# Kernel optimization log

Measured on AMD Instinct MI355X. Metric: run time of the kernel, lower is better.

The kernel has to match this reference:

```python
import math
import jax, jax.numpy as jnp
import numpy as np

B, S, D, H = 4, 2048, 768, 8


def setup_inputs() -> dict:
    key = jax.random.key(0)
    ks = jax.random.split(key, 8)
    x = jax.random.normal(ks[0], (B, S, D), dtype=jnp.float32)
    # padding mask: True = masked position, shape [B, S, 1] as consumed by forward
    attention_mask = jax.random.randint(ks[1], (B, S, 1), 0, 2) == 1
    W_q = jax.random.normal(ks[2], (D, D), dtype=jnp.float32) * 0.02
    b_q = jax.random.normal(ks[3], (D,), dtype=jnp.float32) * 0.02
    W_v = jax.random.normal(ks[4], (D, D), dtype=jnp.float32) * 0.02
    b_v = jax.random.normal(ks[5], (D,), dtype=jnp.float32) * 0.02
    gamma = jnp.ones((D,), dtype=jnp.float32)
    beta = jnp.zeros((D,), dtype=jnp.float32)
    return {"x": x, "attention_mask": attention_mask, "W_q": W_q, "b_q": b_q,
            "W_v": W_v, "b_v": b_v, "gamma": gamma, "beta": beta}


def reference(x, attention_mask, W_q, b_q, W_v, b_v, gamma, beta):
    b, s, d = x.shape
    dk = d // H
    scale = math.sqrt(dk)
    q = (x @ W_q.T + b_q).reshape(b, s, H, dk).transpose(0, 2, 1, 3)  # [B,H,S,dk]
    # faithful to source: k and v BOTH use the V projection (original bug)
    kv = (x @ W_v.T + b_v).reshape(b, s, H, dk).transpose(0, 2, 1, 3)
    k = kv
    v = kv
    weight = jnp.einsum('bhid,bhjd->bhij', q, k) / scale  # [B,H,S,S]
    pad = attention_mask[:, None, :, :]                   # [B,1,S,1] -> broadcast over heads, j
    causal = jnp.triu(jnp.ones((s, s), dtype=bool), 1)    # [S,S]
    mask = pad | causal
    weight = jnp.where(mask, jnp.float32(-1e9), weight)
    # faithful: softmax over dim=2 (the query axis), as in the source
    score = jax.nn.softmax(weight, axis=2)
    out = jnp.einsum('bhij,bhjd->bhid', score, v)         # [B,H,S,dk]
    out = out.transpose(0, 2, 1, 3).reshape(b, s, d)
    out = out + x                                          # residual
    mu = jnp.mean(out, axis=-1, keepdims=True)
    var = jnp.mean((out - mu) ** 2, axis=-1, keepdims=True)
    return (out - mu) / jnp.sqrt(var + 1e-5) * gamma + beta
```

## Files before the change

### kernel.cpp

```cpp
#include <hip/hip_runtime.h>

#define B 4
#define S 2048
#define D 768
#define H 8
#define DK 96
#define NBH (B*H)
#define SD (B*S*D)

typedef __bf16 bf16x8 __attribute__((ext_vector_type(8)));
typedef float f32x4 __attribute__((ext_vector_type(4)));
typedef unsigned short ushort_t;
typedef __attribute__((ext_vector_type(8))) unsigned short ushort8;
typedef __attribute__((ext_vector_type(4))) unsigned short us4;

static constexpr float NEG = -1.0e9f;
static constexpr float SCALE_L2E = 0.14724515567714155f;

__device__ __forceinline__ float exp2v(float x) { return __builtin_amdgcn_exp2f(x); }

__device__ __forceinline__ ushort_t f2bf(float f) {
    union { float f; unsigned u; } v; v.f = f;
    unsigned r = v.u + 0x7fffu + ((v.u >> 16) & 1u);
    return (ushort_t)(r >> 16);
}

__device__ __forceinline__ unsigned cvt_pk(float a, float b) {
    unsigned d;
    asm("v_cvt_pk_bf16_f32 %0, %1, %2" : "=v"(d) : "v"(a), "v"(b));
    return d;
}
__device__ __forceinline__ ushort8 pack8(const float4& a, const float4& b) {
    union { unsigned u[4]; ushort8 s; } r;
    r.u[0] = cvt_pk(a.x, a.y); r.u[1] = cvt_pk(a.z, a.w);
    r.u[2] = cvt_pk(b.x, b.y); r.u[3] = cvt_pk(b.z, b.w);
    return r.s;
}
__device__ __forceinline__ us4 pack4(const float4& a) {
    union { unsigned u[2]; us4 s; } r;
    r.u[0] = cvt_pk(a.x, a.y); r.u[1] = cvt_pk(a.z, a.w);
    return r.s;
}

#define MFMA16(a, b, c) __builtin_amdgcn_mfma_f32_16x16x32_bf16((a), (b), (c), 0, 0, 0)

__global__ __launch_bounds__(256) void convert_bf16(
    const float* __restrict__ wq, const float* __restrict__ wv,
    ushort_t* __restrict__ wqb, ushort_t* __restrict__ wvb)
{
    const int stride = gridDim.x * 256;
    const int idx = blockIdx.x * 256 + threadIdx.x;
    for (int i = idx; i < (D * D) / 4; i += stride) {
        ((us4*)wqb)[i] = pack4(((const float4*)wq)[i]);
        ((us4*)wvb)[i] = pack4(((const float4*)wv)[i]);
    }
}

__global__ __launch_bounds__(256) void in_proj_gemm(
    const float* __restrict__ x,
    const ushort_t* __restrict__ wqb, const float* __restrict__ bq,
    const ushort_t* __restrict__ wvb, const float* __restrict__ bv,
    ushort_t* __restrict__ Qb, ushort_t* __restrict__ KVb,
    ushort_t* __restrict__ KVt)
{
    const ushort_t* __restrict__ Wm = blockIdx.z ? wvb : wqb;
    const float* __restrict__ bia   = blockIdx.z ? bv : bq;
    ushort_t* __restrict__ outp     = blockIdx.z ? KVb : Qb;
    const float osc = blockIdx.z ? 1.0f : SCALE_L2E;

    const int bn = blockIdx.x * 128;
    const int bm = blockIdx.y * 128;
    const int tid = threadIdx.x;
    const int lane = tid & 63;
    const int wid = tid >> 6;
    const int wm = (wid >> 1) * 64, wn = (wid & 1) * 64;
    const int lr = lane & 15, lg = lane >> 4;

    __shared__ __align__(16) ushort_t As[2][128][40];
    __shared__ __align__(16) ushort_t Bs[2][128][40];

    const int r0 = tid >> 2, c8 = (tid & 3) * 8;
    const float*    xg0 = &x [(size_t)(bm + r0) * D + c8];
    const float*    xg1 = xg0 + (size_t)64 * D;
    const ushort_t* wg0 = &Wm[(size_t)(bn + r0) * D + c8];
    const ushort_t* wg1 = wg0 + (size_t)64 * D;

    float4 xv[4];
    ushort8 wv2[2];

    f32x4 acc[4][4];
    #pragma unroll
    for (int m = 0; m < 4; ++m)
        #pragma unroll
        for (int n = 0; n < 4; ++n) acc[m][n] = (f32x4){0.f, 0.f, 0.f, 0.f};

    {
        xv[0] = *(const float4*)(xg0);     xv[1] = *(const float4*)(xg0 + 4);
        xv[2] = *(const float4*)(xg1);     xv[3] = *(const float4*)(xg1 + 4);
        wv2[0] = *(const ushort8*)(wg0);   wv2[1] = *(const ushort8*)(wg1);
        *(ushort8*)&As[0][r0][c8]      = pack8(xv[0], xv[1]);
        *(ushort8*)&As[0][r0 + 64][c8] = pack8(xv[2], xv[3]);
        *(ushort8*)&Bs[0][r0][c8]      = wv2[0];
        *(ushort8*)&Bs[0][r0 + 64][c8] = wv2[1];
    }

    for (int k = 0; k < 24; ++k) {
        __syncthreads();
        const int buf = k & 1;
        if (k < 23) {
            const int ko = (k + 1) * 32;
            xv[0] = *(const float4*)(xg0 + ko);     xv[1] = *(const float4*)(xg0 + ko + 4);
            xv[2] = *(const float4*)(xg1 + ko);     xv[3] = *(const float4*)(xg1 + ko + 4);
            wv2[0] = *(const ushort8*)(wg0 + ko);   wv2[1] = *(const ushort8*)(wg1 + ko);
        }
        bf16x8 a[4], bfr[4];
        #pragma unroll
        for (int m = 0; m < 4; ++m) a[m]   = *(const bf16x8*)&As[buf][wm + m * 16 + lr][lg * 8];
        #pragma unroll
        for (int n = 0; n < 4; ++n) bfr[n] = *(const bf16x8*)&Bs[buf][wn + n * 16 + lr][lg * 8];
        #pragma unroll
        for (int m = 0; m < 4; ++m)
            #pragma unroll
            for (int n = 0; n < 4; ++n)
                acc[m][n] = MFMA16(a[m], bfr[n], acc[m][n]);
        if (k < 23) {
            const int nb = (k + 1) & 1;
            *(ushort8*)&As[nb][r0][c8]      = pack8(xv[0], xv[1]);
            *(ushort8*)&As[nb][r0 + 64][c8] = pack8(xv[2], xv[3]);
            *(ushort8*)&Bs[nb][r0][c8]      = wv2[0];
            *(ushort8*)&Bs[nb][r0 + 64][c8] = wv2[1];
        }
    }

    #pragma unroll
    for (int m = 0; m < 4; ++m) {
        #pragma unroll
        for (int n = 0; n < 4; ++n) {
            int col = bn + wn + n * 16 + lr;
            float bb = bia[col];
            int row0 = bm + wm + m * 16 + lg * 4;
            us4 o;
            #pragma unroll
            for (int r = 0; r < 4; ++r) o[r] = f2bf((acc[m][n][r] + bb) * osc);
            #pragma unroll
            for (int r = 0; r < 4; ++r) outp[(size_t)(row0 + r) * D + col] = o[r];
            if (blockIdx.z) {
                int hh = col / DK, dd = col - hh * DK;
                int bb2 = row0 >> 11, ss = row0 & (S - 1);
                *(us4*)&KVt[((size_t)(bb2 * H + hh) * DK + dd) * S + ss] = o;
            }
        }
    }
}

__global__ __launch_bounds__(256) void col_stats(
    const ushort_t* __restrict__ Qb, const ushort_t* __restrict__ KVb,
    const int* __restrict__ amask,
    float* __restrict__ colM, float* __restrict__ colSinv)
{
    const int bh = blockIdx.y;
    const int jt = (bh & 16) ? (31 - (int)blockIdx.x) : (int)blockIdx.x;
    const int b = bh >> 3, h = bh & 7;
    const int j0 = jt * 64;
    const int tid = threadIdx.x;
    const int lane = tid & 63;
    const int w = tid >> 6;
    const int lr = lane & 15, lg = lane >> 4;

    __shared__ __align__(16) ushort_t qs[2][64][104];
    __shared__ int pads[2][64];

    bf16x8 kf[3];
    #pragma unroll
    for (int ks2 = 0; ks2 < 3; ++ks2)
        kf[ks2] = *(const bf16x8*)&KVb[(size_t)(b * S + j0 + w * 16 + lr) * D + h * DK + ks2 * 32 + lg * 8];

    int kr[3], kc[3];
    const ushort_t* qg[3];
    #pragma unroll
    for (int k3 = 0; k3 < 3; ++k3) {
        int c = tid + k3 * 256;
        kr[k3] = c / 12; kc[k3] = (c % 12) * 8;
        qg[k3] = &Qb[(size_t)(b * S + j0 + kr[k3]) * D + h * DK + kc[k3]];
    }
    const int* pg = amask + b * S + j0 + (tid < 64 ? tid : 0);

    ushort8 pq[3]; int ppad = 0;
    #pragma unroll
    for (int k3 = 0; k3 < 3; ++k3) { pq[k3] = *(const ushort8*)qg[k3]; qg[k3] += (size_t)64 * D; }
    if (tid < 64) { ppad = *pg; }
    pg += 64;

    float m = NEG, ssum = 0.f;
    const int jg = j0 + w * 16 + lr;
    const int nit = (S / 64) - jt;

    for (int t = 0; t < nit; ++t) {
        const int buf = t & 1;
        const int i0 = j0 + t * 64;
        #pragma unroll
        for (int k3 = 0; k3 < 3; ++k3) *(ushort8*)&qs[buf][kr[k3]][kc[k3]] = pq[k3];
        if (tid < 64) pads[buf][tid] = ppad;
        __syncthreads();
        if (t + 1 < nit) {
            #pragma unroll
            for (int k3 = 0; k3 < 3; ++k3) { pq[k3] = *(const ushort8*)qg[k3]; qg[k3] += (size_t)64 * D; }
            if (tid < 64) { ppad = *pg; }
            pg += 64;
        }

        f32x4 dacc[4];
        #pragma unroll
        for (int f = 0; f < 4; ++f) dacc[f] = (f32x4){0.f, 0.f, 0.f, 0.f};
        #pragma unroll
        for (int ks2 = 0; ks2 < 3; ++ks2) {
            #pragma unroll
            for (int f = 0; f < 4; ++f) {
                bf16x8 afr = *(const bf16x8*)&qs[buf][f * 16 + lr][ks2 * 32 + lg * 8];
                dacc[f] = MFMA16(afr, kf[ks2], dacc[f]);
            }
        }

        #pragma unroll
        for (int f = 0; f < 4; ++f) {
            const int ib = f * 16 + lg * 4;
            float wv[4];
            #pragma unroll
            for (int r = 0; r < 4; ++r) {
                int ig = i0 + ib + r;
                wv[r] = (pads[buf][ib + r] != 0 || jg > ig) ? NEG : dacc[f][r];
            }
            float vmax = fmaxf(fmaxf(wv[0], wv[1]), fmaxf(wv[2], wv[3]));
            float mn = fmaxf(m, vmax);
            ssum = ssum * exp2v(m - mn)
                 + exp2v(wv[0] - mn) + exp2v(wv[1] - mn)
                 + exp2v(wv[2] - mn) + exp2v(wv[3] - mn);
            m = mn;
        }
    }

    float m2 = m, s2 = ssum;
    #pragma unroll
    for (int off = 16; off < 64; off <<= 1) {
        float mo = __shfl_xor(m2, off);
        float so = __shfl_xor(s2, off);
        float mn = fmaxf(m2, mo);
        s2 = s2 * exp2v(m2 - mn) + so * exp2v(mo - mn);
        m2 = mn;
    }
    if (lane < 16) {
        if (m2 == NEG) s2 += (float)j0;
        colM[bh * S + jg] = m2;
        colSinv[bh * S + jg] = 1.0f / s2;
    }
}

__global__ __launch_bounds__(256, 4) void attn_pv(
    const ushort_t* __restrict__ Qb, const ushort_t* __restrict__ KVb,
    const ushort_t* __restrict__ KVt,
    const int* __restrict__ amask,
    const float* __restrict__ colM, const float* __restrict__ colSinv,
    const float* __restrict__ x, float* __restrict__ out)
{
    const int bh = blockIdx.y;
    const int it = (bh & 16) ? (31 - (int)blockIdx.x) : (int)blockIdx.x;
    const int b = bh >> 3, h = bh & 7;
    const int i0 = it * 64;
    const int tid = threadIdx.x;
    const int lane = tid & 63;
    const int w = tid >> 6;
    const int lr = lane & 15, lg = lane >> 4;

    __shared__ __align__(16) ushort_t kvs[64][104];
    __shared__ __align__(16) ushort_t kvt[96][88];
    __shared__ __align__(16) ushort_t ps[64][72];
    __shared__ __align__(16) float cm[64];
    __shared__ __align__(16) float csv[64];

    bf16x8 qf[3];
    #pragma unroll
    for (int ks2 = 0; ks2 < 3; ++ks2)
        qf[ks2] = *(const bf16x8*)&Qb[(size_t)(b * S + i0 + w * 16 + lr) * D + h * DK + ks2 * 32 + lg * 8];

    const int my_pad = (int)(amask[b * S + i0 + w * 16 + lr] != 0);
    const int i_g = i0 + w * 16 + lr;

    int kr[3], kc[3], tr[3], tc[3];
    const ushort_t* kvg[3];
    const ushort_t* ktg[3];
    #pragma unroll
    for (int k3 = 0; k3 < 3; ++k3) {
        int c = tid + k3 * 256;
        kr[k3] = c / 12;  kc[k3] = (c % 12) * 8;
        tr[k3] = c >> 3;  tc[k3] = (c & 7) * 8;
        kvg[k3] = &KVb[(size_t)(b * S + kr[k3]) * D + h * DK + kc[k3]];
        ktg[k3] = &KVt[((size_t)(b * H + h) * DK + tr[k3]) * S + tc[k3]];
    }
    const float* cmg  = colM    + (size_t)bh * S + (tid < 64 ? tid : 0);
    const float* csvg = colSinv + (size_t)bh * S + (tid < 64 ? tid : 0);

    ushort8 pkv[3], pkt[3]; float pcm = 0.f, pcsv = 0.f;
    #pragma unroll
    for (int k3 = 0; k3 < 3; ++k3) {
        pkv[k3] = *(const ushort8*)kvg[k3];  kvg[k3] += (size_t)64 * D;
        pkt[k3] = *(const ushort8*)ktg[k3];  ktg[k3] += 64;
    }
    if (tid < 64) { pcm = *cmg; pcsv = *csvg; }
    cmg += 64; csvg += 64;

    f32x4 acc[6];
    #pragma unroll
    for (int df = 0; df < 6; ++df) acc[df] = (f32x4){0.f, 0.f, 0.f, 0.f};

    for (int jt2 = 0; jt2 <= it; ++jt2) {
        const int j0 = jt2 * 64;
        __syncthreads();
        #pragma unroll
        for (int k3 = 0; k3 < 3; ++k3) {
            *(ushort8*)&kvs[kr[k3]][kc[k3]] = pkv[k3];
            *(ushort8*)&kvt[tr[k3]][tc[k3]] = pkt[k3];
        }
        if (tid < 64) { cm[tid] = pcm; csv[tid] = pcsv; }
        __syncthreads();
        if (jt2 < it) {
            #pragma unroll
            for (int k3 = 0; k3 < 3; ++k3) {
                pkv[k3] = *(const ushort8*)kvg[k3];  kvg[k3] += (size_t)64 * D;
                pkt[k3] = *(const ushort8*)ktg[k3];  ktg[k3] += 64;
            }
            if (tid < 64) { pcm = *cmg; pcsv = *csvg; }
            cmg += 64; csvg += 64;
        }

        f32x4 dacc[4];
        #pragma unroll
        for (int jf = 0; jf < 4; ++jf) dacc[jf] = (f32x4){0.f, 0.f, 0.f, 0.f};
        #pragma unroll
        for (int ks2 = 0; ks2 < 3; ++ks2) {
            #pragma unroll
            for (int jf = 0; jf < 4; ++jf) {
                bf16x8 bfr = *(const bf16x8*)&kvs[jf * 16 + lr][ks2 * 32 + lg * 8];
                dacc[jf] = MFMA16(bfr, qf[ks2], dacc[jf]);
            }
        }

        #pragma unroll
        for (int jf = 0; jf < 4; ++jf) {
            const int jbase = jf * 16 + lg * 4;
            f32x4 cmv  = *(const f32x4*)&cm[jbase];
            f32x4 csvv = *(const f32x4*)&csv[jbase];
            float pv[4];
            #pragma unroll
            for (int r = 0; r < 4; ++r) {
                int jgl = j0 + jbase + r;
                bool msk = my_pad || (jgl > i_g);
                float wvv = msk ? NEG : dacc[jf][r];
                pv[r] = exp2v(wvv - cmv[r]) * csvv[r];
            }
            union { unsigned u[2]; uint2 v; } o;
            o.u[0] = cvt_pk(pv[0], pv[1]);
            o.u[1] = cvt_pk(pv[2], pv[3]);
            *(uint2*)&ps[w * 16 + lr][jbase] = o.v;
        }

        #pragma unroll
        for (int ks2 = 0; ks2 < 2; ++ks2) {
            bf16x8 afr = *(const bf16x8*)&ps[w * 16 + lr][ks2 * 32 + lg * 8];
            #pragma unroll
            for (int df = 0; df < 6; ++df) {
                bf16x8 bfr = *(const bf16x8*)&kvt[df * 16 + lr][ks2 * 32 + lg * 8];
                acc[df] = MFMA16(afr, bfr, acc[df]);
            }
        }
    }

    #pragma unroll
    for (int df = 0; df < 6; ++df) {
        int d = h * DK + df * 16 + lr;
        #pragma unroll
        for (int r = 0; r < 4; ++r) {
            size_t gi = (size_t)(b * S + i0 + w * 16 + lg * 4 + r) * D + d;
            out[gi] = acc[df][r] + x[gi];
        }
    }
}

__global__ __launch_bounds__(256) void layer_norm(
    float* __restrict__ out,
    const float* __restrict__ gamma, const float* __restrict__ beta)
{
    const int row = blockIdx.x * 4 + (threadIdx.x >> 6);
    const int lane = threadIdx.x & 63;
    float* o = out + (size_t)row * D;

    float4 v[3];
    #pragma unroll
    for (int p = 0; p < 3; ++p) v[p] = *(const float4*)&o[lane * 4 + p * 256];

    float s = 0.f;
    #pragma unroll
    for (int p = 0; p < 3; ++p) s += v[p].x + v[p].y + v[p].z + v[p].w;
    #pragma unroll
    for (int off = 1; off < 64; off <<= 1) s += __shfl_xor(s, off);
    const float mu = s * (1.0f / D);

    float q = 0.f;
    #pragma unroll
    for (int p = 0; p < 3; ++p) {
        float a = v[p].x - mu, bb = v[p].y - mu, c = v[p].z - mu, dd = v[p].w - mu;
        q += a * a + bb * bb + c * c + dd * dd;
    }
    #pragma unroll
    for (int off = 1; off < 64; off <<= 1) q += __shfl_xor(q, off);
    const float inv = 1.0f / sqrtf(q * (1.0f / D) + 1e-5f);

    #pragma unroll
    for (int p = 0; p < 3; ++p) {
        float4 g = *(const float4*)&gamma[lane * 4 + p * 256];
        float4 bt = *(const float4*)&beta[lane * 4 + p * 256];
        float4 r;
        r.x = (v[p].x - mu) * inv * g.x + bt.x;
        r.y = (v[p].y - mu) * inv * g.y + bt.y;
        r.z = (v[p].z - mu) * inv * g.z + bt.z;
        r.w = (v[p].w - mu) * inv * g.w + bt.w;
        *(float4*)&o[lane * 4 + p * 256] = r;
    }
}

extern "C" void kernel_launch(void* const* d_in, const int* in_sizes, int n_in,
                              void* d_out, int out_size, void* d_ws, size_t ws_size,
                              hipStream_t stream)
{
    const float* x     = (const float*)d_in[0];
    const int*   amask = (const int*)  d_in[1];
    const float* Wq    = (const float*)d_in[2];
    const float* bq    = (const float*)d_in[3];
    const float* Wv    = (const float*)d_in[4];
    const float* bv    = (const float*)d_in[5];
    const float* gamma = (const float*)d_in[6];
    const float* beta  = (const float*)d_in[7];
    float* out = (float*)d_out;

    ushort_t* wqb  = (ushort_t*)d_ws;
    ushort_t* wvb  = wqb + (size_t)D * D;
    ushort_t* Qb   = wvb + (size_t)D * D;
    ushort_t* KVb  = Qb  + (size_t)SD;
    ushort_t* KVt  = KVb + (size_t)SD;
    float* colM    = (float*)(KVt + (size_t)SD);
    float* colSinv = colM + (size_t)NBH * S;

    convert_bf16<<<576, 256, 0, stream>>>(Wq, Wv, wqb, wvb);
    in_proj_gemm<<<dim3(D / 128, (B * S) / 128, 2), 256, 0, stream>>>(
        x, wqb, bq, wvb, bv, Qb, KVb, KVt);
    col_stats<<<dim3(S / 64, NBH), 256, 0, stream>>>(
        Qb, KVb, amask, colM, colSinv);
    attn_pv<<<dim3(S / 64, NBH), 256, 0, stream>>>(
        Qb, KVb, KVt, amask, colM, colSinv, x, out);
    layer_norm<<<(B * S) / 4, 256, 0, stream>>>(out, gamma, beta);
}
```

Measured before the change: 162.0 us.

## Store V in MFMA fragment layout and load PV operands directly from global

```diff
diff --git a/kernel.cpp b/kernel.cpp
--- a/kernel.cpp
+++ b/kernel.cpp
@@ -61,7 +61,7 @@
     const ushort_t* __restrict__ wqb, const float* __restrict__ bq,
     const ushort_t* __restrict__ wvb, const float* __restrict__ bv,
     ushort_t* __restrict__ Qb, ushort_t* __restrict__ KVb,
-    ushort_t* __restrict__ KVt)
+    ushort_t* __restrict__ KVf)
 {
     const ushort_t* __restrict__ Wm = blockIdx.z ? wvb : wqb;
     const float* __restrict__ bia   = blockIdx.z ? bv : bq;
@@ -118,11 +118,13 @@
         for (int m = 0; m < 4; ++m) a[m]   = *(const bf16x8*)&As[buf][wm + m * 16 + lr][lg * 8];
         #pragma unroll
         for (int n = 0; n < 4; ++n) bfr[n] = *(const bf16x8*)&Bs[buf][wn + n * 16 + lr][lg * 8];
+        __builtin_amdgcn_s_setprio(1);
         #pragma unroll
         for (int m = 0; m < 4; ++m)
             #pragma unroll
             for (int n = 0; n < 4; ++n)
                 acc[m][n] = MFMA16(a[m], bfr[n], acc[m][n]);
+        __builtin_amdgcn_s_setprio(0);
         if (k < 23) {
             const int nb = (k + 1) & 1;
             *(ushort8*)&As[nb][r0][c8]      = pack8(xv[0], xv[1]);
@@ -146,8 +148,11 @@
             for (int r = 0; r < 4; ++r) outp[(size_t)(row0 + r) * D + col] = o[r];
             if (blockIdx.z) {
                 int hh = col / DK, dd = col - hh * DK;
-                int bb2 = row0 >> 11, ss = row0 & (S - 1);
-                *(us4*)&KVt[((size_t)(bb2 * H + hh) * DK + dd) * S + ss] = o;
+                int df = dd >> 4, dd15 = dd & 15;
+                int b2 = row0 >> 11, s = row0 & (S - 1);
+                size_t off = ((size_t)(b2 * H + hh) * 6 + df) * 32768
+                           + ((s >> 5) * 512 + ((s >> 3) & 3) * 128 + dd15 * 8 + (s & 7));
+                *(us4*)&KVf[off] = o;
             }
         }
     }
@@ -212,6 +217,7 @@
         f32x4 dacc[4];
         #pragma unroll
         for (int f = 0; f < 4; ++f) dacc[f] = (f32x4){0.f, 0.f, 0.f, 0.f};
+        __builtin_amdgcn_s_setprio(1);
         #pragma unroll
         for (int ks2 = 0; ks2 < 3; ++ks2) {
             #pragma unroll
@@ -220,6 +226,7 @@
                 dacc[f] = MFMA16(afr, kf[ks2], dacc[f]);
             }
         }
+        __builtin_amdgcn_s_setprio(0);
 
         #pragma unroll
         for (int f = 0; f < 4; ++f) {
@@ -257,7 +264,7 @@
 
 __global__ __launch_bounds__(256, 4) void attn_pv(
     const ushort_t* __restrict__ Qb, const ushort_t* __restrict__ KVb,
-    const ushort_t* __restrict__ KVt,
+    const ushort_t* __restrict__ KVf,
     const int* __restrict__ amask,
     const float* __restrict__ colM, const float* __restrict__ colSinv,
     const float* __restrict__ x, float* __restrict__ out)
@@ -272,7 +279,6 @@
     const int lr = lane & 15, lg = lane >> 4;
 
     __shared__ __align__(16) ushort_t kvs[64][104];
-    __shared__ __align__(16) ushort_t kvt[96][88];
     __shared__ __align__(16) ushort_t ps[64][72];
     __shared__ __align__(16) float cm[64];
     __shared__ __align__(16) float csv[64];
@@ -285,25 +291,23 @@
     const int my_pad = (int)(amask[b * S + i0 + w * 16 + lr] != 0);
     const int i_g = i0 + w * 16 + lr;
 
-    int kr[3], kc[3], tr[3], tc[3];
+    int kr[3], kc[3];
     const ushort_t* kvg[3];
-    const ushort_t* ktg[3];
     #pragma unroll
     for (int k3 = 0; k3 < 3; ++k3) {
         int c = tid + k3 * 256;
         kr[k3] = c / 12;  kc[k3] = (c % 12) * 8;
-        tr[k3] = c >> 3;  tc[k3] = (c & 7) * 8;
         kvg[k3] = &KVb[(size_t)(b * S + kr[k3]) * D + h * DK + kc[k3]];
-        ktg[k3] = &KVt[((size_t)(b * H + h) * DK + tr[k3]) * S + tc[k3]];
-    }
+    }
+    const ushort_t* vg = KVf + (size_t)(b * H + h) * 6 * 32768 + (size_t)lane * 8;
+
     const float* cmg  = colM    + (size_t)bh * S + (tid < 64 ? tid : 0);
     const float* csvg = colSinv + (size_t)bh * S + (tid < 64 ? tid : 0);
 
-    ushort8 pkv[3], pkt[3]; float pcm = 0.f, pcsv = 0.f;
+    ushort8 pkv[3]; float pcm = 0.f, pcsv = 0.f;
     #pragma unroll
     for (int k3 = 0; k3 < 3; ++k3) {
         pkv[k3] = *(const ushort8*)kvg[k3];  kvg[k3] += (size_t)64 * D;
-        pkt[k3] = *(const ushort8*)ktg[k3];  ktg[k3] += 64;
     }
     if (tid < 64) { pcm = *cmg; pcsv = *csvg; }
     cmg += 64; csvg += 64;
@@ -316,17 +320,14 @@
         const int j0 = jt2 * 64;
         __syncthreads();
         #pragma unroll
-        for (int k3 = 0; k3 < 3; ++k3) {
+        for (int k3 = 0; k3 < 3; ++k3)
             *(ushort8*)&kvs[kr[k3]][kc[k3]] = pkv[k3];
-            *(ushort8*)&kvt[tr[k3]][tc[k3]] = pkt[k3];
-        }
         if (tid < 64) { cm[tid] = pcm; csv[tid] = pcsv; }
         __syncthreads();
         if (jt2 < it) {
             #pragma unroll
             for (int k3 = 0; k3 < 3; ++k3) {
                 pkv[k3] = *(const ushort8*)kvg[k3];  kvg[k3] += (size_t)64 * D;
-                pkt[k3] = *(const ushort8*)ktg[k3];  ktg[k3] += 64;
             }
             if (tid < 64) { pcm = *cmg; pcsv = *csvg; }
             cmg += 64; csvg += 64;
@@ -335,6 +336,7 @@
         f32x4 dacc[4];
         #pragma unroll
         for (int jf = 0; jf < 4; ++jf) dacc[jf] = (f32x4){0.f, 0.f, 0.f, 0.f};
+        __builtin_amdgcn_s_setprio(1);
         #pragma unroll
         for (int ks2 = 0; ks2 < 3; ++ks2) {
             #pragma unroll
@@ -343,6 +345,7 @@
                 dacc[jf] = MFMA16(bfr, qf[ks2], dacc[jf]);
             }
         }
+        __builtin_amdgcn_s_setprio(0);
 
         #pragma unroll
         for (int jf = 0; jf < 4; ++jf) {
@@ -363,15 +366,18 @@
             *(uint2*)&ps[w * 16 + lr][jbase] = o.v;
         }
 
+        const ushort_t* vit = vg + (size_t)jt2 * 1024;
+        __builtin_amdgcn_s_setprio(1);
         #pragma unroll
         for (int ks2 = 0; ks2 < 2; ++ks2) {
             bf16x8 afr = *(const bf16x8*)&ps[w * 16 + lr][ks2 * 32 + lg * 8];
             #pragma unroll
             for (int df = 0; df < 6; ++df) {
-                bf16x8 bfr = *(const bf16x8*)&kvt[df * 16 + lr][ks2 * 32 + lg * 8];
-                acc[df] = MFMA16(afr, bfr, acc[df]);
-            }
-        }
+                bf16x8 vfr = *(const bf16x8*)(vit + (size_t)df * 32768 + ks2 * 512);
+                acc[df] = MFMA16(afr, vfr, acc[df]);
+            }
+        }
+        __builtin_amdgcn_s_setprio(0);
     }
 
     #pragma unroll
@@ -445,16 +451,16 @@
     ushort_t* wvb  = wqb + (size_t)D * D;
     ushort_t* Qb   = wvb + (size_t)D * D;
     ushort_t* KVb  = Qb  + (size_t)SD;
-    ushort_t* KVt  = KVb + (size_t)SD;
-    float* colM    = (float*)(KVt + (size_t)SD);
+    ushort_t* KVf  = KVb + (size_t)SD;
+    float* colM    = (float*)(KVf + (size_t)SD);
     float* colSinv = colM + (size_t)NBH * S;
 
     convert_bf16<<<576, 256, 0, stream>>>(Wq, Wv, wqb, wvb);
     in_proj_gemm<<<dim3(D / 128, (B * S) / 128, 2), 256, 0, stream>>>(
-        x, wqb, bq, wvb, bv, Qb, KVb, KVt);
+        x, wqb, bq, wvb, bv, Qb, KVb, KVf);
     col_stats<<<dim3(S / 64, NBH), 256, 0, stream>>>(
         Qb, KVb, amask, colM, colSinv);
     attn_pv<<<dim3(S / 64, NBH), 256, 0, stream>>>(
-        Qb, KVb, KVt, amask, colM, colSinv, x, out);
+        Qb, KVb, KVf, amask, colM, colSinv, x, out);
     layer_norm<<<(B * S) / 4, 256, 0, stream>>>(out, gamma, beta);
 }
```

Result: slower. 245.0 us (+51.3%).

## Double attn_pv query tile to 128 rows with 512-thread blocks

Applied to the files above, without the earlier changes.

```diff
diff --git a/kernel.cpp b/kernel.cpp
--- a/kernel.cpp
+++ b/kernel.cpp
@@ -255,7 +255,7 @@
     }
 }
 
-__global__ __launch_bounds__(256, 4) void attn_pv(
+__global__ __launch_bounds__(512, 4) void attn_pv(
     const ushort_t* __restrict__ Qb, const ushort_t* __restrict__ KVb,
     const ushort_t* __restrict__ KVt,
     const int* __restrict__ amask,
@@ -263,9 +263,9 @@
     const float* __restrict__ x, float* __restrict__ out)
 {
     const int bh = blockIdx.y;
-    const int it = (bh & 16) ? (31 - (int)blockIdx.x) : (int)blockIdx.x;
+    const int it = (bh & 16) ? (15 - (int)blockIdx.x) : (int)blockIdx.x;
     const int b = bh >> 3, h = bh & 7;
-    const int i0 = it * 64;
+    const int i0 = it * 128;
     const int tid = threadIdx.x;
     const int lane = tid & 63;
     const int w = tid >> 6;
@@ -273,7 +273,7 @@
 
     __shared__ __align__(16) ushort_t kvs[64][104];
     __shared__ __align__(16) ushort_t kvt[96][88];
-    __shared__ __align__(16) ushort_t ps[64][72];
+    __shared__ __align__(16) ushort_t ps[128][72];
     __shared__ __align__(16) float cm[64];
     __shared__ __align__(16) float csv[64];
 
@@ -285,26 +285,31 @@
     const int my_pad = (int)(amask[b * S + i0 + w * 16 + lr] != 0);
     const int i_g = i0 + w * 16 + lr;
 
-    int kr[3], kc[3], tr[3], tc[3];
-    const ushort_t* kvg[3];
-    const ushort_t* ktg[3];
+    ushort_t* ldst[3];
+    const ushort_t* gsrc[3];
+    size_t gstr[3];
     #pragma unroll
     for (int k3 = 0; k3 < 3; ++k3) {
-        int c = tid + k3 * 256;
-        kr[k3] = c / 12;  kc[k3] = (c % 12) * 8;
-        tr[k3] = c >> 3;  tc[k3] = (c & 7) * 8;
-        kvg[k3] = &KVb[(size_t)(b * S + kr[k3]) * D + h * DK + kc[k3]];
-        ktg[k3] = &KVt[((size_t)(b * H + h) * DK + tr[k3]) * S + tc[k3]];
+        int c = tid + k3 * 512;
+        if (c < 768) {
+            int r = c / 12, cc = (c % 12) * 8;
+            ldst[k3] = &kvs[r][cc];
+            gsrc[k3] = &KVb[(size_t)(b * S + r) * D + h * DK + cc];
+            gstr[k3] = (size_t)64 * D;
+        } else {
+            int c2 = c - 768;
+            int r = c2 >> 3, cc = (c2 & 7) * 8;
+            ldst[k3] = &kvt[r][cc];
+            gsrc[k3] = &KVt[((size_t)(b * H + h) * DK + r) * S + cc];
+            gstr[k3] = 64;
+        }
     }
     const float* cmg  = colM    + (size_t)bh * S + (tid < 64 ? tid : 0);
     const float* csvg = colSinv + (size_t)bh * S + (tid < 64 ? tid : 0);
 
-    ushort8 pkv[3], pkt[3]; float pcm = 0.f, pcsv = 0.f;
-    #pragma unroll
-    for (int k3 = 0; k3 < 3; ++k3) {
-        pkv[k3] = *(const ushort8*)kvg[k3];  kvg[k3] += (size_t)64 * D;
-        pkt[k3] = *(const ushort8*)ktg[k3];  ktg[k3] += 64;
-    }
+    ushort8 pk[3]; float pcm = 0.f, pcsv = 0.f;
+    #pragma unroll
+    for (int k3 = 0; k3 < 3; ++k3) { pk[k3] = *(const ushort8*)gsrc[k3]; gsrc[k3] += gstr[k3]; }
     if (tid < 64) { pcm = *cmg; pcsv = *csvg; }
     cmg += 64; csvg += 64;
 
@@ -312,22 +317,18 @@
     #pragma unroll
     for (int df = 0; df < 6; ++df) acc[df] = (f32x4){0.f, 0.f, 0.f, 0.f};
 
-    for (int jt2 = 0; jt2 <= it; ++jt2) {
+    const int nj = 2 * it + 2;
+    for (int jt2 = 0; jt2 < nj; ++jt2) {
         const int j0 = jt2 * 64;
         __syncthreads();
         #pragma unroll
-        for (int k3 = 0; k3 < 3; ++k3) {
-            *(ushort8*)&kvs[kr[k3]][kc[k3]] = pkv[k3];
-            *(ushort8*)&kvt[tr[k3]][tc[k3]] = pkt[k3];
-        }
+        for (int k3 = 0; k3 < 3; ++k3)
+            *(ushort8*)ldst[k3] = pk[k3];
         if (tid < 64) { cm[tid] = pcm; csv[tid] = pcsv; }
         __syncthreads();
-        if (jt2 < it) {
-            #pragma unroll
-            for (int k3 = 0; k3 < 3; ++k3) {
-                pkv[k3] = *(const ushort8*)kvg[k3];  kvg[k3] += (size_t)64 * D;
-                pkt[k3] = *(const ushort8*)ktg[k3];  ktg[k3] += 64;
-            }
+        if (jt2 + 1 < nj) {
+            #pragma unroll
+            for (int k3 = 0; k3 < 3; ++k3) { pk[k3] = *(const ushort8*)gsrc[k3]; gsrc[k3] += gstr[k3]; }
             if (tid < 64) { pcm = *cmg; pcsv = *csvg; }
             cmg += 64; csvg += 64;
         }
@@ -454,7 +455,7 @@
         x, wqb, bq, wvb, bv, Qb, KVb, KVt);
     col_stats<<<dim3(S / 64, NBH), 256, 0, stream>>>(
         Qb, KVb, amask, colM, colSinv);
-    attn_pv<<<dim3(S / 64, NBH), 256, 0, stream>>>(
+    attn_pv<<<dim3(16, 32), 512, 0, stream>>>(
         Qb, KVb, KVt, amask, colM, colSinv, x, out);
     layer_norm<<<(B * S) / 4, 256, 0, stream>>>(out, gamma, beta);
 }
```

Result: faster. 158.5 us (median of 3 runs) (-2.1%).
